# Performance work log

Hardware: AMD Instinct MI355X
Metric: run time of the kernel (lower is better)

## Reference

```python
import jax, jax.numpy as jnp
import numpy as np

B, C, N = 4, 256, 4096
CQ = C // 4

def setup_inputs() -> dict:
    key = jax.random.key(0)
    ks = jax.random.split(key, 8)
    inputs = jax.random.normal(ks[0], (B, C, N), dtype=jnp.float32)
    # Conv1d(kernel=1) == pointwise linear over channels: weight [out_c, in_c], bias [out_c]
    sc = 1.0 / np.sqrt(C)
    wq = jax.random.uniform(ks[1], (CQ, C), jnp.float32, -sc, sc)
    bq = jax.random.uniform(ks[2], (CQ,), jnp.float32, -sc, sc)
    wk = jax.random.uniform(ks[3], (CQ, C), jnp.float32, -sc, sc)
    bk = jax.random.uniform(ks[4], (CQ,), jnp.float32, -sc, sc)
    wv = jax.random.uniform(ks[5], (C, C), jnp.float32, -sc, sc)
    bv = jax.random.uniform(ks[6], (C,), jnp.float32, -sc, sc)
    gamma = jax.random.normal(ks[7], (1,), jnp.float32) * 0.1  # nonzero so attention path is exercised
    return {"inputs": inputs, "wq": wq, "bq": bq, "wk": wk, "bk": bk, "wv": wv, "bv": bv, "gamma": gamma}

def reference(inputs, wq, bq, wk, bk, wv, bv, gamma):
    # pointwise conv1d projections: [B,C,N] -> [B,out_c,N]
    q = jnp.einsum('oc,bcn->bon', wq, inputs) + bq[None, :, None]   # [B,CQ,N]
    k = jnp.einsum('oc,bcn->bon', wk, inputs) + bk[None, :, None]   # [B,CQ,N]
    v = jnp.einsum('oc,bcn->bon', wv, inputs) + bv[None, :, None]   # [B,C,N]
    # s = q^T k : [B,N,N] (no scaling, as in the source)
    s = jnp.einsum('bon,bom->bnm', q, k)
    beta = jax.nn.softmax(s, axis=-1)
    # o = v @ beta : [B,C,N]
    o = jnp.einsum('bcn,bnm->bcm', v, beta)
    return gamma * o + inputs
```

## Files before the change

kernel.cpp:

```cpp
#include <hip/hip_runtime.h>

#define NB   4
#define C_IN 256
#define CQD  64
#define NPT  4096
#define L2E  1.44269504088896f

typedef __attribute__((ext_vector_type(8))) short bf16x8;
typedef __attribute__((ext_vector_type(4))) float f32x4;
typedef unsigned short u16;
typedef unsigned int   u32;

#define EXP2F(x)      __builtin_amdgcn_exp2f(x)
#define MFMA32(A,B,C) __builtin_amdgcn_mfma_f32_16x16x32_bf16(A,B,C,0,0,0)

__device__ __forceinline__ u16 f2bf(float f) {
    u32 u = __float_as_uint(f);
    u += 0x7fff + ((u >> 16) & 1);
    return (u16)(u >> 16);
}
__device__ __forceinline__ u32 pack_trunc(float lo, float hi) {
    return __builtin_amdgcn_perm(__float_as_uint(hi), __float_as_uint(lo), 0x07060302u);
}


__global__ void prep_kernel(
    const float* __restrict__ wq, const float* __restrict__ bq,
    const float* __restrict__ wk, const float* __restrict__ bk,
    const float* __restrict__ wv, const float* __restrict__ bv,
    u16* __restrict__ wbf, float* __restrict__ bias)
{
    const int gid = blockIdx.x*256 + threadIdx.x;
    if (gid < 384*256) {
        const int r = gid >> 8, c = gid & 255;
        const float v = (r < 64) ? wq[r*256 + c]
                      : (r < 128) ? wk[(r-64)*256 + c]
                                  : wv[(r-128)*256 + c];
        wbf[gid] = f2bf(v);
    } else if (gid < 384*256 + 384) {
        const int r = gid - 384*256;
        bias[r] = (r < 64) ? bq[r] : (r < 128) ? bk[r-64] : bv[r-128];
    }
}

union ProjShared {
    u16 x_t[32][264];
    struct { u16 qk[32][136]; u16 vl[256][40]; } ep;
};

__global__ __launch_bounds__(256) void proj_kernel(
    const float* __restrict__ x, const u16* __restrict__ wbf,
    const float* __restrict__ bias,
    u16* __restrict__ qF, u16* __restrict__ kF, u16* __restrict__ vF)
{
    __shared__ ProjShared sh;

    const int t  = threadIdx.x;
    const int n0 = blockIdx.x * 32;
    const int b  = blockIdx.y;

    {
        const int ln = t & 31;
        const int cg = t >> 5;
        #pragma unroll
        for (int rr = 0; rr < 8; rr++) {
            const int c = 4*cg + 32*rr;
            const float f0 = x[((size_t)(b*C_IN + c+0))*NPT + n0 + ln];
            const float f1 = x[((size_t)(b*C_IN + c+1))*NPT + n0 + ln];
            const float f2 = x[((size_t)(b*C_IN + c+2))*NPT + n0 + ln];
            const float f3 = x[((size_t)(b*C_IN + c+3))*NPT + n0 + ln];
            ushort4 u4;
            u4.x = f2bf(f0); u4.y = f2bf(f1); u4.z = f2bf(f2); u4.w = f2bf(f3);
            *(ushort4*)&sh.x_t[ln][c] = u4;
        }
    }
    __syncthreads();

    const int w = t >> 6, l = t & 63, q = l >> 4, c16 = l & 15;

    f32x4 acc[6][2];
    #pragma unroll
    for (int ot = 0; ot < 6; ot++)
        #pragma unroll
        for (int nt = 0; nt < 2; nt++)
            acc[ot][nt] = (f32x4){0.f, 0.f, 0.f, 0.f};

    #pragma unroll
    for (int kk = 0; kk < 8; kk++) {
        const bf16x8 bf0 = *(const bf16x8*)&sh.x_t[c16     ][kk*32 + 8*q];
        const bf16x8 bf1 = *(const bf16x8*)&sh.x_t[16 + c16][kk*32 + 8*q];
        #pragma unroll
        for (int ot = 0; ot < 6; ot++) {
            const int o = 16*(4*ot + w) + c16;
            const bf16x8 af = *(const bf16x8*)&wbf[(size_t)o*C_IN + kk*32 + 8*q];
            acc[ot][0] = MFMA32(af, bf0, acc[ot][0]);
            acc[ot][1] = MFMA32(af, bf1, acc[ot][1]);
        }
    }
    __syncthreads();

    #pragma unroll
    for (int ot = 0; ot < 6; ot++) {
        const int T  = 4*ot + w;
        const int ob = 16*T + 4*q;
        float b0 = bias[ob+0], b1 = bias[ob+1], b2 = bias[ob+2], b3 = bias[ob+3];
        #pragma unroll
        for (int nt = 0; nt < 2; nt++) {
            const f32x4 a = acc[ot][nt];
            const float v0 = a[0]+b0, v1 = a[1]+b1, v2 = a[2]+b2, v3 = a[3]+b3;
            if (ot < 2) {
                uint2 u;
                u.x = (u32)f2bf(v0) | ((u32)f2bf(v1) << 16);
                u.y = (u32)f2bf(v2) | ((u32)f2bf(v3) << 16);
                *(uint2*)&sh.ep.qk[16*nt + c16][16*T + 4*q] = u;
            } else {
                const int cb = 16*T - 128 + 4*q;
                sh.ep.vl[cb+0][16*nt + c16] = f2bf(v0);
                sh.ep.vl[cb+1][16*nt + c16] = f2bf(v1);
                sh.ep.vl[cb+2][16*nt + c16] = f2bf(v2);
                sh.ep.vl[cb+3][16*nt + c16] = f2bf(v3);
            }
        }
    }
    __syncthreads();

    {
        const int n    = t >> 3;
        const int c    = t & 7;
        const int g    = (n0 + n) >> 4;
        const int lane = 16*(c & 3) + (n & 15);
        const size_t dq = ((size_t)(b*256 + g))*1024 + (size_t)(c >> 2)*512 + lane*8;
        *(uint4*)&qF[dq] = *(uint4*)&sh.ep.qk[n][8*c];
        *(uint4*)&kF[dq] = *(uint4*)&sh.ep.qk[n][64 + 8*c];
        const int cg   = t >> 4, c16v = t & 15;
        const int ng   = n0 >> 5;
        u16* vdst = &vF[(((size_t)(b*16 + cg))*128 + ng)*512 + c16v*8];
        #pragma unroll
        for (int j = 0; j < 4; j++)
            *(uint4*)&vdst[j*128] = *(uint4*)&sh.ep.vl[t][8*j];
    }
}

__global__ __launch_bounds__(256, 4) void stats_kernel(
    const u16* __restrict__ qF, const u16* __restrict__ kF,
    float* __restrict__ psum)
{
    const int t = threadIdx.x;
    const int w = t >> 6, l = t & 63, q = l >> 4, c16 = l & 15;
    const int ms = blockIdx.x, nt = blockIdx.y, b = blockIdx.z;
    const int nb = nt*64 + 16*w;

    const u16* qp = &qF[((size_t)(b*256 + nt*4 + w))*1024 + l*8];
    const bf16x8 aq0 = *(const bf16x8*)qp;
    const bf16x8 aq1 = *(const bf16x8*)(qp + 512);

    float rz[4] = {0.f, 0.f, 0.f, 0.f};

    const int mbeg = ms*1024, mend = mbeg + 1024;
    const u16* kbase = &kF[((size_t)b*256)*1024 + l*8];

    bf16x8 kc0[4], kc1[4];
    #pragma unroll
    for (int mj = 0; mj < 4; mj++) {
        const u16* kp = kbase + (size_t)((mbeg >> 4) + mj)*1024;
        kc0[mj] = *(const bf16x8*)kp;
        kc1[mj] = *(const bf16x8*)(kp + 512);
    }

    for (int m0 = mbeg; m0 < mend; m0 += 64) {
        const int mn = (m0 + 64 < mend) ? m0 + 64 : mbeg;
        bf16x8 kn0[4], kn1[4];
        #pragma unroll
        for (int mj = 0; mj < 4; mj++) {
            const u16* kp = kbase + (size_t)((mn >> 4) + mj)*1024;
            kn0[mj] = *(const bf16x8*)kp;
            kn1[mj] = *(const bf16x8*)(kp + 512);
        }

        f32x4 s[4];
        #pragma unroll
        for (int mj = 0; mj < 4; mj++) {
            f32x4 a = {0.f, 0.f, 0.f, 0.f};
            a = MFMA32(aq0, kc0[mj], a);
            a = MFMA32(aq1, kc1[mj], a);
            s[mj] = a;
        }
        #pragma unroll
        for (int r = 0; r < 4; r++) {
            rz[r] += EXP2F(s[0][r]*L2E) + EXP2F(s[1][r]*L2E)
                   + EXP2F(s[2][r]*L2E) + EXP2F(s[3][r]*L2E);
        }
        #pragma unroll
        for (int mj = 0; mj < 4; mj++) {
            kc0[mj] = kn0[mj];
            kc1[mj] = kn1[mj];
        }
    }
    #pragma unroll
    for (int r = 0; r < 4; r++) {
        float Z = rz[r];
        #pragma unroll
        for (int d = 1; d < 16; d <<= 1) Z += __shfl_xor(Z, d, 64);
        if (c16 == 0)
            psum[((size_t)(b*4 + ms))*NPT + nb + 4*q + r] = Z;
    }
}

__global__ void merge_kernel(const float* __restrict__ psum, float* __restrict__ Lrow)
{
    const int g = blockIdx.x*256 + threadIdx.x;
    const int b = g >> 12;
    const int n = g & 4095;
    float Z = 0.f;
    #pragma unroll
    for (int s = 0; s < 4; s++) Z += psum[((size_t)(b*4+s))*NPT + n];
    Lrow[(size_t)b*NPT + n] = __log2f(Z);
}

__global__ __launch_bounds__(512, 2) void attn_kernel(
    const u16* __restrict__ qF, const u16* __restrict__ kF, const u16* __restrict__ vF,
    const float* __restrict__ Lrow, const float* __restrict__ gamma,
    const float* __restrict__ x, float* __restrict__ out)
{
    __shared__ uint2 p_l[2][2176];

    const int t = threadIdx.x;
    const int w = t >> 6, l = t & 63, q = l >> 4, c16 = l & 15;

    const int id  = blockIdx.x;
    const int xcd = id & 7;
    const int jb  = id >> 3;
    const int b   = xcd >> 1;
    const int mt  = ((xcd & 1) << 5) | jb;
    const int m0  = mt * 64;

    bf16x8 kf[4][2];
    #pragma unroll
    for (int mj = 0; mj < 4; mj++) {
        const u16* kp = &kF[((size_t)(b*256 + mt*4 + mj))*1024 + l*8];
        kf[mj][0] = *(const bf16x8*)kp;
        kf[mj][1] = *(const bf16x8*)(kp + 512);
    }

    f32x4 acc[2][4];
    #pragma unroll
    for (int cg = 0; cg < 2; cg++)
        #pragma unroll
        for (int mj = 0; mj < 4; mj++)
            acc[cg][mj] = (f32x4){0.f, 0.f, 0.f, 0.f};

    const u16*   qbase  = &qF[((size_t)(b*256 + w))*1024 + l*8];
    const u16*   vbase0 = &vF[(((size_t)(b*16 + 2*w))*128)*512 + l*8];
    const u16*   vbase1 = vbase0 + (size_t)128*512;
    const float* Lb     = &Lrow[(size_t)b*NPT + 16*w + 4*q];

    const int Uw  = (w*16 + q*4)*17 + c16;
    const int Ur0 = ((q>>1)*16 + (q&1)*8)*17 + c16;

    bf16x8 qa0 = *(const bf16x8*)qbase;
    bf16x8 qa1 = *(const bf16x8*)(qbase + 512);

    bf16x8 vac0[4], vac1[4];
    #pragma unroll
    for (int kc = 0; kc < 4; kc++) {
        vac0[kc] = *(const bf16x8*)(vbase0 + (size_t)kc*512);
        vac1[kc] = *(const bf16x8*)(vbase1 + (size_t)kc*512);
    }
    float4 Lrc = *(const float4*)Lb;

    int buf = 0;
    for (int nt = 0; nt < 32; nt++) {
        const int n0  = nt * 128;
        const int ntn = (nt < 31) ? nt + 1 : nt;

        f32x4 s[4];
        #pragma unroll
        for (int mj = 0; mj < 4; mj++) {
            f32x4 a = {0.f, 0.f, 0.f, 0.f};
            a = MFMA32(qa0, kf[mj][0], a);
            a = MFMA32(qa1, kf[mj][1], a);
            s[mj] = a;
        }
        if (nt < 31) {
            qa0 = *(const bf16x8*)(qbase + (size_t)(nt+1)*8192);
            qa1 = *(const bf16x8*)(qbase + (size_t)(nt+1)*8192 + 512);
        }
        bf16x8 van0[4], van1[4];
        #pragma unroll
        for (int kc = 0; kc < 4; kc++) {
            van0[kc] = *(const bf16x8*)(vbase0 + (size_t)(ntn*4 + kc)*512);
            van1[kc] = *(const bf16x8*)(vbase1 + (size_t)(ntn*4 + kc)*512);
        }
        const float4 Lrn = *(const float4*)(Lb + ntn*128);

        #pragma unroll
        for (int mj = 0; mj < 4; mj++) {
            const float p0 = EXP2F(s[mj][0]*L2E - Lrc.x);
            const float p1 = EXP2F(s[mj][1]*L2E - Lrc.y);
            const float p2 = EXP2F(s[mj][2]*L2E - Lrc.z);
            const float p3 = EXP2F(s[mj][3]*L2E - Lrc.w);
            uint2 u;
            u.x = pack_trunc(p0, p1);
            u.y = pack_trunc(p2, p3);
            p_l[buf][Uw + mj*17] = u;
        }
        __syncthreads();

        __builtin_amdgcn_s_setprio(1);
        #pragma unroll
        for (int mj = 0; mj < 4; mj++) {
            #pragma unroll
            for (int kc = 0; kc < 4; kc++) {
                const uint2 u0 = p_l[buf][Ur0 + kc*544 + mj*17];
                const uint2 u1 = p_l[buf][Ur0 + kc*544 + mj*17 + 68];
                uint4 f = make_uint4(u0.x, u0.y, u1.x, u1.y);
                const bf16x8 pf = *(bf16x8*)&f;
                acc[0][mj] = MFMA32(vac0[kc], pf, acc[0][mj]);
                acc[1][mj] = MFMA32(vac1[kc], pf, acc[1][mj]);
            }
        }
        __builtin_amdgcn_s_setprio(0);

        #pragma unroll
        for (int kc = 0; kc < 4; kc++) {
            vac0[kc] = van0[kc];
            vac1[kc] = van1[kc];
        }
        Lrc = Lrn;
        buf ^= 1;
    }

    const float g = gamma[0];
    #pragma unroll
    for (int cg = 0; cg < 2; cg++)
        #pragma unroll
        for (int mj = 0; mj < 4; mj++)
            #pragma unroll
            for (int r = 0; r < 4; r++) {
                const size_t o = ((size_t)(b*C_IN + 32*w + 16*cg + 4*q + r))*NPT
                               + m0 + 16*mj + c16;
                out[o] = g*acc[cg][mj][r] + x[o];
            }
}

extern "C" void kernel_launch(void* const* d_in, const int* in_sizes, int n_in,
                              void* d_out, int out_size, void* d_ws, size_t ws_size,
                              hipStream_t stream)
{
    const float* x     = (const float*)d_in[0];
    const float* wq    = (const float*)d_in[1];
    const float* bq    = (const float*)d_in[2];
    const float* wk    = (const float*)d_in[3];
    const float* bk    = (const float*)d_in[4];
    const float* wv    = (const float*)d_in[5];
    const float* bv    = (const float*)d_in[6];
    const float* gamma = (const float*)d_in[7];
    float* out = (float*)d_out;

    u16* qF  = (u16*)d_ws;
    u16* kF  = qF  + (size_t)NB*NPT*CQD;
    u16* vF  = kF  + (size_t)NB*NPT*CQD;
    u16* wbf = vF  + (size_t)NB*C_IN*NPT;
    float* fp    = (float*)(wbf + 384*256);
    float* bias  = fp;
    float* psum  = bias + 384;
    float* Lrow  = psum + (size_t)NB*4*NPT;

    prep_kernel<<<dim3(386), 256, 0, stream>>>(wq, bq, wk, bk, wv, bv, wbf, bias);
    proj_kernel<<<dim3(NPT/32, NB), 256, 0, stream>>>(x, wbf, bias, qF, kF, vF);
    stats_kernel<<<dim3(4, NPT/64, NB), 256, 0, stream>>>(qF, kF, psum);
    merge_kernel<<<dim3(64), 256, 0, stream>>>(psum, Lrow);
    attn_kernel<<<dim3(256), 512, 0, stream>>>(qF, kF, vF, Lrow, gamma, x, out);
}
```

Baseline: 171.7 us.

## Split attention key loop across two wave groups and double stats rows per wave

The attention kernel now runs 1024 threads per block. Two halves of eight waves each process alternate 128-column n tiles, and their accumulators are reduced through shared memory before the epilogue. The explicit register prefetch of the next q/v tiles is removed. The stats kernel now has each wave compute two 16-row groups against the same loaded k fragments, halving the number of k loads per row, and drops its k prefetch. The aim is more latency hiding through extra waves and reuse of k fragments. The cost is a large shared reduction buffer, an extra barrier, possibly lower occupancy, and exposed load latency without prefetch.

```diff
diff --git a/kernel.cpp b/kernel.cpp
--- a/kernel.cpp
+++ b/kernel.cpp
@@ -148,62 +148,53 @@
     const int t = threadIdx.x;
     const int w = t >> 6, l = t & 63, q = l >> 4, c16 = l & 15;
     const int ms = blockIdx.x, nt = blockIdx.y, b = blockIdx.z;
-    const int nb = nt*64 + 16*w;
-
-    const u16* qp = &qF[((size_t)(b*256 + nt*4 + w))*1024 + l*8];
-    const bf16x8 aq0 = *(const bf16x8*)qp;
-    const bf16x8 aq1 = *(const bf16x8*)(qp + 512);
-
-    float rz[4] = {0.f, 0.f, 0.f, 0.f};
-
-    const int mbeg = ms*1024, mend = mbeg + 1024;
+
+    bf16x8 aq[2][2];
+    #pragma unroll
+    for (int j = 0; j < 2; j++) {
+        const u16* qp = &qF[((size_t)(b*256 + nt*8 + 2*w + j))*1024 + l*8];
+        aq[j][0] = *(const bf16x8*)qp;
+        aq[j][1] = *(const bf16x8*)(qp + 512);
+    }
+
+    float rz[2][4] = {{0.f,0.f,0.f,0.f},{0.f,0.f,0.f,0.f}};
     const u16* kbase = &kF[((size_t)b*256)*1024 + l*8];
 
-    bf16x8 kc0[4], kc1[4];
-    #pragma unroll
-    for (int mj = 0; mj < 4; mj++) {
-        const u16* kp = kbase + (size_t)((mbeg >> 4) + mj)*1024;
-        kc0[mj] = *(const bf16x8*)kp;
-        kc1[mj] = *(const bf16x8*)(kp + 512);
-    }
-
-    for (int m0 = mbeg; m0 < mend; m0 += 64) {
-        const int mn = (m0 + 64 < mend) ? m0 + 64 : mbeg;
-        bf16x8 kn0[4], kn1[4];
+    for (int m0 = ms*1024; m0 < ms*1024 + 1024; m0 += 64) {
+        bf16x8 k0[4], k1[4];
         #pragma unroll
         for (int mj = 0; mj < 4; mj++) {
-            const u16* kp = kbase + (size_t)((mn >> 4) + mj)*1024;
-            kn0[mj] = *(const bf16x8*)kp;
-            kn1[mj] = *(const bf16x8*)(kp + 512);
-        }
-
-        f32x4 s[4];
-        #pragma unroll
-        for (int mj = 0; mj < 4; mj++) {
-            f32x4 a = {0.f, 0.f, 0.f, 0.f};
-            a = MFMA32(aq0, kc0[mj], a);
-            a = MFMA32(aq1, kc1[mj], a);
-            s[mj] = a;
-        }
+            const u16* kp = kbase + (size_t)((m0 >> 4) + mj)*1024;
+            k0[mj] = *(const bf16x8*)kp;
+            k1[mj] = *(const bf16x8*)(kp + 512);
+        }
+        #pragma unroll
+        for (int j = 0; j < 2; j++) {
+            f32x4 s[4];
+            #pragma unroll
+            for (int mj = 0; mj < 4; mj++) {
+                f32x4 a = {0.f, 0.f, 0.f, 0.f};
+                a = MFMA32(aq[j][0], k0[mj], a);
+                a = MFMA32(aq[j][1], k1[mj], a);
+                s[mj] = a;
+            }
+            #pragma unroll
+            for (int r = 0; r < 4; r++) {
+                rz[j][r] += EXP2F(s[0][r]*L2E) + EXP2F(s[1][r]*L2E)
+                          + EXP2F(s[2][r]*L2E) + EXP2F(s[3][r]*L2E);
+            }
+        }
+    }
+    #pragma unroll
+    for (int j = 0; j < 2; j++)
         #pragma unroll
         for (int r = 0; r < 4; r++) {
-            rz[r] += EXP2F(s[0][r]*L2E) + EXP2F(s[1][r]*L2E)
-                   + EXP2F(s[2][r]*L2E) + EXP2F(s[3][r]*L2E);
-        }
-        #pragma unroll
-        for (int mj = 0; mj < 4; mj++) {
-            kc0[mj] = kn0[mj];
-            kc1[mj] = kn1[mj];
-        }
-    }
-    #pragma unroll
-    for (int r = 0; r < 4; r++) {
-        float Z = rz[r];
-        #pragma unroll
-        for (int d = 1; d < 16; d <<= 1) Z += __shfl_xor(Z, d, 64);
-        if (c16 == 0)
-            psum[((size_t)(b*4 + ms))*NPT + nb + 4*q + r] = Z;
-    }
+            float Z = rz[j][r];
+            #pragma unroll
+            for (int d = 1; d < 16; d <<= 1) Z += __shfl_xor(Z, d, 64);
+            if (c16 == 0)
+                psum[((size_t)(b*4 + ms))*NPT + nt*128 + 32*w + 16*j + 4*q + r] = Z;
+        }
 }
 
 __global__ void merge_kernel(const float* __restrict__ psum, float* __restrict__ Lrow)
@@ -217,15 +208,17 @@
     Lrow[(size_t)b*NPT + n] = __log2f(Z);
 }
 
-__global__ __launch_bounds__(512, 2) void attn_kernel(
+__global__ __launch_bounds__(1024, 4) void attn_kernel(
     const u16* __restrict__ qF, const u16* __restrict__ kF, const u16* __restrict__ vF,
     const float* __restrict__ Lrow, const float* __restrict__ gamma,
     const float* __restrict__ x, float* __restrict__ out)
 {
-    __shared__ uint2 p_l[2][2176];
+    __shared__ uint2 p_l[2][2][2176];
+    __shared__ float red[16640];
 
     const int t = threadIdx.x;
     const int w = t >> 6, l = t & 63, q = l >> 4, c16 = l & 15;
+    const int sub = w >> 3, wl = w & 7;
 
     const int id  = blockIdx.x;
     const int xcd = id & 7;
@@ -249,29 +242,18 @@
         for (int mj = 0; mj < 4; mj++)
             acc[cg][mj] = (f32x4){0.f, 0.f, 0.f, 0.f};
 
-    const u16*   qbase  = &qF[((size_t)(b*256 + w))*1024 + l*8];
-    const u16*   vbase0 = &vF[(((size_t)(b*16 + 2*w))*128)*512 + l*8];
+    const u16*   qbase  = &qF[((size_t)(b*256 + sub*8 + wl))*1024 + l*8];
+    const u16*   vbase0 = &vF[(((size_t)(b*16 + 2*wl))*128 + 4*sub)*512 + l*8];
     const u16*   vbase1 = vbase0 + (size_t)128*512;
-    const float* Lb     = &Lrow[(size_t)b*NPT + 16*w + 4*q];
-
-    const int Uw  = (w*16 + q*4)*17 + c16;
+    const float* Lb     = &Lrow[(size_t)b*NPT + sub*128 + 16*wl + 4*q];
+
+    const int Uw  = (wl*16 + q*4)*17 + c16;
     const int Ur0 = ((q>>1)*16 + (q&1)*8)*17 + c16;
 
-    bf16x8 qa0 = *(const bf16x8*)qbase;
-    bf16x8 qa1 = *(const bf16x8*)(qbase + 512);
-
-    bf16x8 vac0[4], vac1[4];
-    #pragma unroll
-    for (int kc = 0; kc < 4; kc++) {
-        vac0[kc] = *(const bf16x8*)(vbase0 + (size_t)kc*512);
-        vac1[kc] = *(const bf16x8*)(vbase1 + (size_t)kc*512);
-    }
-    float4 Lrc = *(const float4*)Lb;
-
     int buf = 0;
-    for (int nt = 0; nt < 32; nt++) {
-        const int n0  = nt * 128;
-        const int ntn = (nt < 31) ? nt + 1 : nt;
+    for (int nt = 0; nt < 16; nt++) {
+        const bf16x8 qa0 = *(const bf16x8*)(qbase + (size_t)nt*16384);
+        const bf16x8 qa1 = *(const bf16x8*)(qbase + (size_t)nt*16384 + 512);
 
         f32x4 s[4];
         #pragma unroll
@@ -281,66 +263,70 @@
             a = MFMA32(qa1, kf[mj][1], a);
             s[mj] = a;
         }
-        if (nt < 31) {
-            qa0 = *(const bf16x8*)(qbase + (size_t)(nt+1)*8192);
-            qa1 = *(const bf16x8*)(qbase + (size_t)(nt+1)*8192 + 512);
-        }
-        bf16x8 van0[4], van1[4];
+        bf16x8 va0[4], va1[4];
         #pragma unroll
         for (int kc = 0; kc < 4; kc++) {
-            van0[kc] = *(const bf16x8*)(vbase0 + (size_t)(ntn*4 + kc)*512);
-            van1[kc] = *(const bf16x8*)(vbase1 + (size_t)(ntn*4 + kc)*512);
-        }
-        const float4 Lrn = *(const float4*)(Lb + ntn*128);
+            va0[kc] = *(const bf16x8*)(vbase0 + (size_t)(8*nt + kc)*512);
+            va1[kc] = *(const bf16x8*)(vbase1 + (size_t)(8*nt + kc)*512);
+        }
+        const float4 Lr = *(const float4*)(Lb + nt*256);
 
         #pragma unroll
         for (int mj = 0; mj < 4; mj++) {
-            const float p0 = EXP2F(s[mj][0]*L2E - Lrc.x);
-            const float p1 = EXP2F(s[mj][1]*L2E - Lrc.y);
-            const float p2 = EXP2F(s[mj][2]*L2E - Lrc.z);
-            const float p3 = EXP2F(s[mj][3]*L2E - Lrc.w);
+            const float p0 = EXP2F(s[mj][0]*L2E - Lr.x);
+            const float p1 = EXP2F(s[mj][1]*L2E - Lr.y);
+            const float p2 = EXP2F(s[mj][2]*L2E - Lr.z);
+            const float p3 = EXP2F(s[mj][3]*L2E - Lr.w);
             uint2 u;
             u.x = pack_trunc(p0, p1);
             u.y = pack_trunc(p2, p3);
-            p_l[buf][Uw + mj*17] = u;
+            p_l[buf][sub][Uw + mj*17] = u;
         }
         __syncthreads();
 
+        const uint2* tp = p_l[buf][sub];
         __builtin_amdgcn_s_setprio(1);
         #pragma unroll
         for (int mj = 0; mj < 4; mj++) {
             #pragma unroll
             for (int kc = 0; kc < 4; kc++) {
-                const uint2 u0 = p_l[buf][Ur0 + kc*544 + mj*17];
-                const uint2 u1 = p_l[buf][Ur0 + kc*544 + mj*17 + 68];
+                const uint2 u0 = tp[Ur0 + kc*544 + mj*17];
+                const uint2 u1 = tp[Ur0 + kc*544 + mj*17 + 68];
                 uint4 f = make_uint4(u0.x, u0.y, u1.x, u1.y);
                 const bf16x8 pf = *(bf16x8*)&f;
-                acc[0][mj] = MFMA32(vac0[kc], pf, acc[0][mj]);
-                acc[1][mj] = MFMA32(vac1[kc], pf, acc[1][mj]);
+                acc[0][mj] = MFMA32(va0[kc], pf, acc[0][mj]);
+                acc[1][mj] = MFMA32(va1[kc], pf, acc[1][mj]);
             }
         }
         __builtin_amdgcn_s_setprio(0);
-
-        #pragma unroll
-        for (int kc = 0; kc < 4; kc++) {
-            vac0[kc] = van0[kc];
-            vac1[kc] = van1[kc];
-        }
-        Lrc = Lrn;
         buf ^= 1;
     }
 
-    const float g = gamma[0];
-    #pragma unroll
-    for (int cg = 0; cg < 2; cg++)
-        #pragma unroll
-        for (int mj = 0; mj < 4; mj++)
-            #pragma unroll
-            for (int r = 0; r < 4; r++) {
-                const size_t o = ((size_t)(b*C_IN + 32*w + 16*cg + 4*q + r))*NPT
-                               + m0 + 16*mj + c16;
-                out[o] = g*acc[cg][mj][r] + x[o];
-            }
+    if (sub == 1) {
+        #pragma unroll
+        for (int cg = 0; cg < 2; cg++)
+            #pragma unroll
+            for (int mj = 0; mj < 4; mj++)
+                #pragma unroll
+                for (int r = 0; r < 4; r++)
+                    red[((cg*4 + mj)*4 + r)*520 + wl*64 + l] = acc[cg][mj][r];
+    }
+    __syncthreads();
+    if (sub == 0) {
+        const float g = gamma[0];
+        #pragma unroll
+        for (int cg = 0; cg < 2; cg++)
+            #pragma unroll
+            for (int mj = 0; mj < 4; mj++)
+                #pragma unroll
+                for (int r = 0; r < 4; r++) {
+                    const float v = acc[cg][mj][r]
+                                  + red[((cg*4 + mj)*4 + r)*520 + wl*64 + l];
+                    const size_t o = ((size_t)(b*C_IN + 32*wl + 16*cg + 4*q + r))*NPT
+                                   + m0 + 16*mj + c16;
+                    out[o] = g*v + x[o];
+                }
+    }
 }
 
 extern "C" void kernel_launch(void* const* d_in, const int* in_sizes, int n_in,
@@ -368,7 +354,7 @@
 
     prep_kernel<<<dim3(386), 256, 0, stream>>>(wq, bq, wk, bk, wv, bv, wbf, bias);
     proj_kernel<<<dim3(NPT/32, NB), 256, 0, stream>>>(x, wbf, bias, qF, kF, vF);
-    stats_kernel<<<dim3(4, NPT/64, NB), 256, 0, stream>>>(qF, kF, psum);
+    stats_kernel<<<dim3(4, NPT/128, NB), 256, 0, stream>>>(qF, kF, psum);
     merge_kernel<<<dim3(64), 256, 0, stream>>>(psum, Lrow);
-    attn_kernel<<<dim3(256), 512, 0, stream>>>(qF, kF, vF, Lrow, gamma, x, out);
-}
+    attn_kernel<<<dim3(256), 1024, 0, stream>>>(qF, kF, vF, Lrow, gamma, x, out);
+}
```

New measurement: 166.6 us. 2.9% less time.

## Software-pipeline attention loop and double row-tiles per warp in stats kernel

Applied to the files above, without the earlier changes.

The attention kernel is restructured so the QK^T scores and exponentials for the next tile are computed and written to the alternate LDS buffer while the current tile's PV MFMAs run, with a prologue and epilogue, and the setprio hints are removed. This aims to overlap exp/VALU work with matrix work and drop one barrier stall per iteration. Separately, the stats kernel now has each warp handle two 16-row query tiles, reusing every loaded K fragment twice and halving the grid. The stats kernel's register prefetch of the next K tile is dropped, which may expose load latency.

```diff
diff --git a/kernel.cpp b/kernel.cpp
--- a/kernel.cpp
+++ b/kernel.cpp
@@ -148,62 +148,53 @@
     const int t = threadIdx.x;
     const int w = t >> 6, l = t & 63, q = l >> 4, c16 = l & 15;
     const int ms = blockIdx.x, nt = blockIdx.y, b = blockIdx.z;
-    const int nb = nt*64 + 16*w;
-
-    const u16* qp = &qF[((size_t)(b*256 + nt*4 + w))*1024 + l*8];
-    const bf16x8 aq0 = *(const bf16x8*)qp;
-    const bf16x8 aq1 = *(const bf16x8*)(qp + 512);
-
-    float rz[4] = {0.f, 0.f, 0.f, 0.f};
-
-    const int mbeg = ms*1024, mend = mbeg + 1024;
+
+    bf16x8 aq[2][2];
+    #pragma unroll
+    for (int j = 0; j < 2; j++) {
+        const u16* qp = &qF[((size_t)(b*256 + nt*8 + 2*w + j))*1024 + l*8];
+        aq[j][0] = *(const bf16x8*)qp;
+        aq[j][1] = *(const bf16x8*)(qp + 512);
+    }
+
+    float rz[2][4] = {{0.f,0.f,0.f,0.f},{0.f,0.f,0.f,0.f}};
     const u16* kbase = &kF[((size_t)b*256)*1024 + l*8];
 
-    bf16x8 kc0[4], kc1[4];
-    #pragma unroll
-    for (int mj = 0; mj < 4; mj++) {
-        const u16* kp = kbase + (size_t)((mbeg >> 4) + mj)*1024;
-        kc0[mj] = *(const bf16x8*)kp;
-        kc1[mj] = *(const bf16x8*)(kp + 512);
-    }
-
-    for (int m0 = mbeg; m0 < mend; m0 += 64) {
-        const int mn = (m0 + 64 < mend) ? m0 + 64 : mbeg;
-        bf16x8 kn0[4], kn1[4];
-        #pragma unroll
-        for (int mj = 0; mj < 4; mj++) {
-            const u16* kp = kbase + (size_t)((mn >> 4) + mj)*1024;
-            kn0[mj] = *(const bf16x8*)kp;
-            kn1[mj] = *(const bf16x8*)(kp + 512);
-        }
-
-        f32x4 s[4];
-        #pragma unroll
-        for (int mj = 0; mj < 4; mj++) {
-            f32x4 a = {0.f, 0.f, 0.f, 0.f};
-            a = MFMA32(aq0, kc0[mj], a);
-            a = MFMA32(aq1, kc1[mj], a);
-            s[mj] = a;
-        }
+    for (int m0 = ms*1024; m0 < ms*1024 + 1024; m0 += 64) {
+        bf16x8 k0[4], k1[4];
+        #pragma unroll
+        for (int mj = 0; mj < 4; mj++) {
+            const u16* kp = kbase + (size_t)((m0 >> 4) + mj)*1024;
+            k0[mj] = *(const bf16x8*)kp;
+            k1[mj] = *(const bf16x8*)(kp + 512);
+        }
+        #pragma unroll
+        for (int j = 0; j < 2; j++) {
+            f32x4 s[4];
+            #pragma unroll
+            for (int mj = 0; mj < 4; mj++) {
+                f32x4 a = {0.f, 0.f, 0.f, 0.f};
+                a = MFMA32(aq[j][0], k0[mj], a);
+                a = MFMA32(aq[j][1], k1[mj], a);
+                s[mj] = a;
+            }
+            #pragma unroll
+            for (int r = 0; r < 4; r++) {
+                rz[j][r] += EXP2F(s[0][r]*L2E) + EXP2F(s[1][r]*L2E)
+                          + EXP2F(s[2][r]*L2E) + EXP2F(s[3][r]*L2E);
+            }
+        }
+    }
+    #pragma unroll
+    for (int j = 0; j < 2; j++)
         #pragma unroll
         for (int r = 0; r < 4; r++) {
-            rz[r] += EXP2F(s[0][r]*L2E) + EXP2F(s[1][r]*L2E)
-                   + EXP2F(s[2][r]*L2E) + EXP2F(s[3][r]*L2E);
-        }
-        #pragma unroll
-        for (int mj = 0; mj < 4; mj++) {
-            kc0[mj] = kn0[mj];
-            kc1[mj] = kn1[mj];
-        }
-    }
-    #pragma unroll
-    for (int r = 0; r < 4; r++) {
-        float Z = rz[r];
-        #pragma unroll
-        for (int d = 1; d < 16; d <<= 1) Z += __shfl_xor(Z, d, 64);
-        if (c16 == 0)
-            psum[((size_t)(b*4 + ms))*NPT + nb + 4*q + r] = Z;
-    }
+            float Z = rz[j][r];
+            #pragma unroll
+            for (int d = 1; d < 16; d <<= 1) Z += __shfl_xor(Z, d, 64);
+            if (c16 == 0)
+                psum[((size_t)(b*4 + ms))*NPT + nt*128 + 32*w + 16*j + 4*q + r] = Z;
+        }
 }
 
 __global__ void merge_kernel(const float* __restrict__ psum, float* __restrict__ Lrow)
@@ -259,7 +250,6 @@
 
     bf16x8 qa0 = *(const bf16x8*)qbase;
     bf16x8 qa1 = *(const bf16x8*)(qbase + 512);
-
     bf16x8 vac0[4], vac1[4];
     #pragma unroll
     for (int kc = 0; kc < 4; kc++) {
@@ -267,12 +257,7 @@
         vac1[kc] = *(const bf16x8*)(vbase1 + (size_t)kc*512);
     }
     float4 Lrc = *(const float4*)Lb;
-
-    int buf = 0;
-    for (int nt = 0; nt < 32; nt++) {
-        const int n0  = nt * 128;
-        const int ntn = (nt < 31) ? nt + 1 : nt;
-
+    {
         f32x4 s[4];
         #pragma unroll
         for (int mj = 0; mj < 4; mj++) {
@@ -281,18 +266,6 @@
             a = MFMA32(qa1, kf[mj][1], a);
             s[mj] = a;
         }
-        if (nt < 31) {
-            qa0 = *(const bf16x8*)(qbase + (size_t)(nt+1)*8192);
-            qa1 = *(const bf16x8*)(qbase + (size_t)(nt+1)*8192 + 512);
-        }
-        bf16x8 van0[4], van1[4];
-        #pragma unroll
-        for (int kc = 0; kc < 4; kc++) {
-            van0[kc] = *(const bf16x8*)(vbase0 + (size_t)(ntn*4 + kc)*512);
-            van1[kc] = *(const bf16x8*)(vbase1 + (size_t)(ntn*4 + kc)*512);
-        }
-        const float4 Lrn = *(const float4*)(Lb + ntn*128);
-
         #pragma unroll
         for (int mj = 0; mj < 4; mj++) {
             const float p0 = EXP2F(s[mj][0]*L2E - Lrc.x);
@@ -302,11 +275,24 @@
             uint2 u;
             u.x = pack_trunc(p0, p1);
             u.y = pack_trunc(p2, p3);
-            p_l[buf][Uw + mj*17] = u;
-        }
+            p_l[0][Uw + mj*17] = u;
+        }
+    }
+    qa0 = *(const bf16x8*)(qbase + 8192);
+    qa1 = *(const bf16x8*)(qbase + 8192 + 512);
+    Lrc = *(const float4*)(Lb + 128);
+
+    int buf = 0;
+    for (int nt = 0; nt < 31; nt++) {
         __syncthreads();
-
-        __builtin_amdgcn_s_setprio(1);
+        f32x4 s[4];
+        #pragma unroll
+        for (int mj = 0; mj < 4; mj++) {
+            f32x4 a = {0.f, 0.f, 0.f, 0.f};
+            a = MFMA32(qa0, kf[mj][0], a);
+            a = MFMA32(qa1, kf[mj][1], a);
+            s[mj] = a;
+        }
         #pragma unroll
         for (int mj = 0; mj < 4; mj++) {
             #pragma unroll
@@ -319,8 +305,28 @@
                 acc[1][mj] = MFMA32(vac1[kc], pf, acc[1][mj]);
             }
         }
-        __builtin_amdgcn_s_setprio(0);
-
+        const int n2 = (nt < 30) ? nt + 2 : 31;
+        qa0 = *(const bf16x8*)(qbase + (size_t)n2*8192);
+        qa1 = *(const bf16x8*)(qbase + (size_t)n2*8192 + 512);
+        bf16x8 van0[4], van1[4];
+        #pragma unroll
+        for (int kc = 0; kc < 4; kc++) {
+            van0[kc] = *(const bf16x8*)(vbase0 + (size_t)((nt+1)*4 + kc)*512);
+            van1[kc] = *(const bf16x8*)(vbase1 + (size_t)((nt+1)*4 + kc)*512);
+        }
+        const float4 Lrn = *(const float4*)(Lb + (size_t)n2*128);
+
+        #pragma unroll
+        for (int mj = 0; mj < 4; mj++) {
+            const float p0 = EXP2F(s[mj][0]*L2E - Lrc.x);
+            const float p1 = EXP2F(s[mj][1]*L2E - Lrc.y);
+            const float p2 = EXP2F(s[mj][2]*L2E - Lrc.z);
+            const float p3 = EXP2F(s[mj][3]*L2E - Lrc.w);
+            uint2 u;
+            u.x = pack_trunc(p0, p1);
+            u.y = pack_trunc(p2, p3);
+            p_l[buf^1][Uw + mj*17] = u;
+        }
         #pragma unroll
         for (int kc = 0; kc < 4; kc++) {
             vac0[kc] = van0[kc];
@@ -328,6 +334,19 @@
         }
         Lrc = Lrn;
         buf ^= 1;
+    }
+    __syncthreads();
+    #pragma unroll
+    for (int mj = 0; mj < 4; mj++) {
+        #pragma unroll
+        for (int kc = 0; kc < 4; kc++) {
+            const uint2 u0 = p_l[buf][Ur0 + kc*544 + mj*17];
+            const uint2 u1 = p_l[buf][Ur0 + kc*544 + mj*17 + 68];
+            uint4 f = make_uint4(u0.x, u0.y, u1.x, u1.y);
+            const bf16x8 pf = *(bf16x8*)&f;
+            acc[0][mj] = MFMA32(vac0[kc], pf, acc[0][mj]);
+            acc[1][mj] = MFMA32(vac1[kc], pf, acc[1][mj]);
+        }
     }
 
     const float g = gamma[0];
@@ -368,7 +387,7 @@
 
     prep_kernel<<<dim3(386), 256, 0, stream>>>(wq, bq, wk, bk, wv, bv, wbf, bias);
     proj_kernel<<<dim3(NPT/32, NB), 256, 0, stream>>>(x, wbf, bias, qF, kF, vF);
-    stats_kernel<<<dim3(4, NPT/64, NB), 256, 0, stream>>>(qF, kF, psum);
+    stats_kernel<<<dim3(4, NPT/128, NB), 256, 0, stream>>>(qF, kF, psum);
     merge_kernel<<<dim3(64), 256, 0, stream>>>(psum, Lrow);
     attn_kernel<<<dim3(256), 512, 0, stream>>>(qF, kF, vF, Lrow, gamma, x, out);
 }
```

New measurement: 163.6 us. -4.7%, faster.
